# Kernel optimization log

Hardware: AMD Instinct MI355X
Metric: run time of the kernel (lower is better)

The kernel has to match this reference:

```python
import jax, jax.numpy as jnp
import numpy as np

# Grid parameters (from init_kwargs)
GRID_W, GRID_L, GRID_H = 96, 96, 48
VOXEL_SIZE = 0.05
MIN_POINTS_PER_VOXEL = 10


def setup_inputs() -> dict:
    key = jax.random.key(0)
    k1, k2 = jax.random.split(key, 2)
    # points uniform over a ~[0,1.5]^3 sub-volume so voxel occupancy is realistic
    point_coordinates = jax.random.uniform(k1, (4, 3, 480, 640), jnp.float32) * 1.5
    point_attributes = jax.random.normal(k2, (4, 16, 480, 640), jnp.float32)
    origin = jnp.zeros((4, 3), jnp.float32)
    return {"point_coordinates": point_coordinates,
            "point_attributes": point_attributes,
            "origin": origin}


def _voxelize_one(coords, attrs, org):
    # coords: [3, N], attrs: [C, N], org: [3]
    V = GRID_W * GRID_L * GRID_H
    bounds = jnp.array([GRID_W, GRID_L, GRID_H], jnp.int32)
    # per-point voxel index (floor == .long() for positive; OOB handled by mask)
    idx3 = jnp.floor((coords - org[:, None]) / VOXEL_SIZE).astype(jnp.int32)  # [3, N]
    in_bounds = jnp.all((idx3 >= 0) & (idx3 < bounds[:, None]), axis=0)       # [N]
    flat = idx3[0] * (GRID_L * GRID_H) + idx3[1] * GRID_H + idx3[2]           # [N]
    flat = jnp.where(in_bounds, flat, 0)  # route OOB points to voxel 0, masked out
    # occupancy: scatter-add of in-bounds mask
    counts = jax.ops.segment_sum(in_bounds.astype(jnp.float32), flat, num_segments=V)
    # max-pool of attributes per voxel; OOB points contribute -inf
    masked = jnp.where(in_bounds[None, :], attrs, -jnp.inf)                   # [C, N]
    vmax = jax.ops.segment_max(masked.T, flat, num_segments=V).T              # [C, V]
    occ = counts >= MIN_POINTS_PER_VOXEL                                      # [V]
    data = jnp.where(occ[None, :] & jnp.isfinite(vmax), vmax, 0.0)            # [C, V]
    return data, occ


def reference(point_coordinates, point_attributes, origin):
    b, c = point_attributes.shape[:2]
    coords = point_coordinates.reshape(b, 3, -1)   # [B, 3, N]
    attrs = point_attributes.reshape(b, c, -1)     # [B, C, N]
    data, occ = jax.vmap(_voxelize_one)(coords, attrs, origin)
    voxeldata = data.reshape(b, c, GRID_W, GRID_L, GRID_H)
    voxeloccupancy = occ.reshape(b, 1, GRID_W, GRID_L, GRID_H).astype(jnp.float32)
    return voxeldata, voxeloccupancy
```

## Files before the change

kernel.cpp:

```cpp
#include <hip/hip_runtime.h>
#include <cstdint>
#include <math.h>

#define GRID_W 96
#define GRID_L 96
#define GRID_H 48
#define NVOX (GRID_W * GRID_L * GRID_H)
#define VOXEL_SIZE 0.05f
#define MIN_PTS 10
#define BATCH 4
#define CHANS 16
#define NPTS (480 * 640)
#define TOTPTS (BATCH * NPTS)
#define TOTVOX (BATCH * NVOX)

#define SCAN_BLKS 864
#define SCAN_TPB 256
#define SCAN_EPT 8
#define SCAN_CHUNK (SCAN_TPB * SCAN_EPT)

#define ROWW 8

typedef unsigned nt_uint4  __attribute__((ext_vector_type(4)));
typedef float    nt_float4 __attribute__((ext_vector_type(4)));
typedef float    nt_float2 __attribute__((ext_vector_type(2)));

#define WS_OFFSETS 0
#define WS_VR      ((TOTVOX + 4) * 4)
#define WS_IDS     (WS_VR + TOTPTS * 4)
#define WS_ROWS    (WS_IDS + TOTPTS * 4 + 16)
#define WS_SUMS    (WS_ROWS + (size_t)TOTPTS * ROWW * 4)
#define WS_NEEDED  ((size_t)(WS_SUMS + 4096))

__device__ __forceinline__ unsigned bf16_rtne(float f) {
    unsigned u = __float_as_uint(f);
    return (u + 0x7FFFu + ((u >> 16) & 1u)) >> 16;
}
__device__ __forceinline__ unsigned pack2(float lo, float hi) {
    return bf16_rtne(lo) | (bf16_rtne(hi) << 16);
}



__global__ void k_pack(const float* __restrict__ attrs,
                       unsigned*    __restrict__ rows)
{
    int t = blockIdx.x * blockDim.x + threadIdx.x;
    if (t >= TOTPTS / 2) return;
    int pid = t * 2;
    int b = pid / NPTS;
    int n = pid - b * NPTS;

    const float* ab = attrs + (size_t)b * CHANS * NPTS + n;
    unsigned w[2][ROWW];
    #pragma unroll
    for (int c = 0; c < CHANS; c += 2) {
        nt_float2 a0 = __builtin_nontemporal_load((const nt_float2*)(ab + (size_t)c * NPTS));
        nt_float2 a1 = __builtin_nontemporal_load((const nt_float2*)(ab + (size_t)(c + 1) * NPTS));
        w[0][c >> 1] = pack2(a0.x, a1.x);
        w[1][c >> 1] = pack2(a0.y, a1.y);
    }
    uint4* dst = (uint4*)(rows + (size_t)pid * ROWW);
    dst[0] = uint4{w[0][0], w[0][1], w[0][2], w[0][3]};
    dst[1] = uint4{w[0][4], w[0][5], w[0][6], w[0][7]};
    dst[2] = uint4{w[1][0], w[1][1], w[1][2], w[1][3]};
    dst[3] = uint4{w[1][4], w[1][5], w[1][6], w[1][7]};
}

__global__ void k_vox(const float* __restrict__ coords,
                      const float* __restrict__ origin,
                      unsigned*    __restrict__ vr,
                      unsigned*    __restrict__ cnt)
{
    int t = blockIdx.x * blockDim.x + threadIdx.x;
    if (t >= TOTPTS / 4) return;
    int pid = t * 4;
    int b = pid / NPTS;
    int n = pid - b * NPTS;

    const float* cb = coords + (size_t)b * 3 * NPTS;
    nt_float4 X = __builtin_nontemporal_load((const nt_float4*)(cb + n));
    nt_float4 Y = __builtin_nontemporal_load((const nt_float4*)(cb + NPTS + n));
    nt_float4 Z = __builtin_nontemporal_load((const nt_float4*)(cb + 2 * NPTS + n));
    float ox = origin[b * 3 + 0];
    float oy = origin[b * 3 + 1];
    float oz = origin[b * 3 + 2];

    float xs[4] = {X.x, X.y, X.z, X.w};
    float ys[4] = {Y.x, Y.y, Y.z, Y.w};
    float zs[4] = {Z.x, Z.y, Z.z, Z.w};

    int  vv[4];
    bool ib[4];
    #pragma unroll
    for (int k = 0; k < 4; ++k) {
        int ix = (int)floorf((xs[k] - ox) / VOXEL_SIZE);
        int iy = (int)floorf((ys[k] - oy) / VOXEL_SIZE);
        int iz = (int)floorf((zs[k] - oz) / VOXEL_SIZE);
        ib[k] = ((unsigned)ix < GRID_W) & ((unsigned)iy < GRID_L) & ((unsigned)iz < GRID_H);
        vv[k] = b * NVOX + ix * (GRID_L * GRID_H) + iy * GRID_H + iz;
    }
    unsigned ps[4];
    #pragma unroll
    for (int k = 0; k < 4; ++k) {
        unsigned p = 0xFFFFFFFFu;
        if (ib[k]) {
            unsigned r = atomicAdd(&cnt[vv[k]], 1u);
            p = ((unsigned)vv[k] << 10) | (r & 1023u);
        }
        ps[k] = p;
    }
    *(uint4*)(vr + pid) = uint4{ps[0], ps[1], ps[2], ps[3]};
}

__global__ void k_scan1(unsigned* __restrict__ offsets,
                        unsigned* __restrict__ sums,
                        float*    __restrict__ occ)
{
    __shared__ unsigned s[SCAN_TPB];
    int t = threadIdx.x;
    int base = blockIdx.x * SCAN_CHUNK + t * SCAN_EPT;

    uint4 a = ((const uint4*)(offsets + base))[0];
    uint4 c = ((const uint4*)(offsets + base))[1];
    unsigned e[SCAN_EPT] = {a.x, a.y, a.z, a.w, c.x, c.y, c.z, c.w};

    nt_float4 oc0, oc1;
    oc0.x = (e[0] >= MIN_PTS) ? 1.f : 0.f;  oc0.y = (e[1] >= MIN_PTS) ? 1.f : 0.f;
    oc0.z = (e[2] >= MIN_PTS) ? 1.f : 0.f;  oc0.w = (e[3] >= MIN_PTS) ? 1.f : 0.f;
    oc1.x = (e[4] >= MIN_PTS) ? 1.f : 0.f;  oc1.y = (e[5] >= MIN_PTS) ? 1.f : 0.f;
    oc1.z = (e[6] >= MIN_PTS) ? 1.f : 0.f;  oc1.w = (e[7] >= MIN_PTS) ? 1.f : 0.f;
    __builtin_nontemporal_store(oc0, ((nt_float4*)(occ + base)));
    __builtin_nontemporal_store(oc1, ((nt_float4*)(occ + base)) + 1);

    unsigned tot = 0;
    #pragma unroll
    for (int k = 0; k < SCAN_EPT; ++k) { unsigned v = e[k]; e[k] = tot; tot += v; }

    s[t] = tot;
    __syncthreads();
    #pragma unroll
    for (int off = 1; off < SCAN_TPB; off <<= 1) {
        unsigned v = (t >= off) ? s[t - off] : 0u;
        __syncthreads();
        s[t] += v;
        __syncthreads();
    }
    unsigned prefix = s[t] - tot;
    #pragma unroll
    for (int k = 0; k < SCAN_EPT; ++k) e[k] += prefix;

    ((uint4*)(offsets + base))[0] = uint4{e[0], e[1], e[2], e[3]};
    ((uint4*)(offsets + base))[1] = uint4{e[4], e[5], e[6], e[7]};

    if (t == SCAN_TPB - 1) sums[blockIdx.x] = s[t];
}

__global__ void k_scan2(unsigned* __restrict__ sums) {
    __shared__ unsigned s[1024];
    int t = threadIdx.x;
    unsigned my = (t < SCAN_BLKS) ? sums[t] : 0u;
    s[t] = my;
    __syncthreads();
    #pragma unroll
    for (int off = 1; off < 1024; off <<= 1) {
        unsigned v = (t >= off) ? s[t - off] : 0u;
        __syncthreads();
        s[t] += v;
        __syncthreads();
    }
    if (t < SCAN_BLKS) sums[t] = s[t] - my;
    if (t == SCAN_BLKS - 1) sums[SCAN_BLKS] = s[t];
}

__global__ void k_scatter_ids4(const unsigned* __restrict__ vr,
                               const unsigned* __restrict__ offsets,
                               const unsigned* __restrict__ sums,
                               int*            __restrict__ ids)
{
    int t = blockIdx.x * blockDim.x + threadIdx.x;
    if (t >= TOTPTS / 4) return;
    int pid = t * 4;
    uint4 P = *(const uint4*)(vr + pid);
    unsigned ps[4] = {P.x, P.y, P.z, P.w};
    #pragma unroll
    for (int k = 0; k < 4; ++k) {
        if (ps[k] != 0xFFFFFFFFu) {
            unsigned v = ps[k] >> 10;
            unsigned pos = offsets[v] + sums[v >> 11] + (ps[k] & 1023u);
            ids[pos] = pid + k;
        }
    }
}

__global__ void k_gather_ind2(const unsigned* __restrict__ rows,
                              const int*      __restrict__ ids,
                              const unsigned* __restrict__ offsets,
                              const unsigned* __restrict__ sums,
                              float*          __restrict__ data)
{
    int g = blockIdx.x * blockDim.x + threadIdx.x;
    if (g >= TOTVOX / 2) return;
    int vox0 = g * 2;

    uint2 O = *(const uint2*)(offsets + vox0);
    unsigned base = sums[vox0 >> 11];
    unsigned s[3];
    s[0] = O.x + base;
    s[1] = O.y + base;
    s[2] = offsets[vox0 + 2] + sums[(vox0 + 2) >> 11];

    float m[2][CHANS];
    #pragma unroll
    for (int q = 0; q < 2; ++q) {
        unsigned k = s[q + 1] - s[q];
        unsigned s0 = s[q];
        if (k >= MIN_PTS) {
            const float ninf = -__builtin_inff();
            #pragma unroll
            for (int c = 0; c < CHANS; ++c) m[q][c] = ninf;
            unsigned j = 0;
            for (; j + 2 <= k; j += 2) {
                int p0 = ids[s0 + j];
                int p1 = ids[s0 + j + 1];
                const uint4* r0p = (const uint4*)(rows + (size_t)p0 * ROWW);
                const uint4* r1p = (const uint4*)(rows + (size_t)p1 * ROWW);
                uint4 l0 = r0p[0], h0 = r0p[1];
                uint4 l1 = r1p[0], h1 = r1p[1];
                unsigned wa[8] = {l0.x, l0.y, l0.z, l0.w, h0.x, h0.y, h0.z, h0.w};
                unsigned wb[8] = {l1.x, l1.y, l1.z, l1.w, h1.x, h1.y, h1.z, h1.w};
                #pragma unroll
                for (int h = 0; h < 8; ++h) {
                    m[q][2 * h]     = fmaxf(m[q][2 * h],
                                        fmaxf(__uint_as_float(wa[h] << 16),
                                              __uint_as_float(wb[h] << 16)));
                    m[q][2 * h + 1] = fmaxf(m[q][2 * h + 1],
                                        fmaxf(__uint_as_float(wa[h] & 0xFFFF0000u),
                                              __uint_as_float(wb[h] & 0xFFFF0000u)));
                }
            }
            if (j < k) {
                int p0 = ids[s0 + j];
                const uint4* r0p = (const uint4*)(rows + (size_t)p0 * ROWW);
                uint4 l0 = r0p[0], h0 = r0p[1];
                unsigned wa[8] = {l0.x, l0.y, l0.z, l0.w, h0.x, h0.y, h0.z, h0.w};
                #pragma unroll
                for (int h = 0; h < 8; ++h) {
                    m[q][2 * h]     = fmaxf(m[q][2 * h], __uint_as_float(wa[h] << 16));
                    m[q][2 * h + 1] = fmaxf(m[q][2 * h + 1],
                                            __uint_as_float(wa[h] & 0xFFFF0000u));
                }
            }
            #pragma unroll
            for (int c = 0; c < CHANS; ++c) if (!isfinite(m[q][c])) m[q][c] = 0.f;
        } else {
            #pragma unroll
            for (int c = 0; c < CHANS; ++c) m[q][c] = 0.f;
        }
    }

    int b = vox0 / NVOX;
    int v0 = vox0 - b * NVOX;
    float* db = data + (size_t)b * CHANS * NVOX + v0;
    #pragma unroll
    for (int c = 0; c < CHANS; ++c) {
        nt_float2 o = {m[0][c], m[1][c]};
        __builtin_nontemporal_store(o, (nt_float2*)(db + (size_t)c * NVOX));
    }
}


__device__ __forceinline__ unsigned flip_f32(float f) {
    unsigned u = __float_as_uint(f);
    unsigned mask = (unsigned)(-(int)(u >> 31)) | 0x80000000u;
    return u ^ mask;
}
__device__ __forceinline__ float unflip_f32(unsigned u) {
    unsigned mask = ((u >> 31) - 1u) | 0x80000000u;
    return __uint_as_float(u ^ mask);
}
#define FLIP_NEG_INF 0x007FFFFFu

__global__ void pv_init(uint4* __restrict__ out) {
    const int DATA4 = BATCH * CHANS * NVOX / 4;
    const int TOT4  = BATCH * (CHANS + 1) * NVOX / 4;
    int i = blockIdx.x * blockDim.x + threadIdx.x;
    if (i < TOT4) {
        unsigned val = (i < DATA4) ? FLIP_NEG_INF : 0u;
        out[i] = uint4{val, val, val, val};
    }
}

__global__ void pv_scatter(const float* __restrict__ coords,
                           const float* __restrict__ attrs,
                           const float* __restrict__ origin,
                           unsigned*    __restrict__ data_u,
                           unsigned*    __restrict__ cnt)
{
    int id = blockIdx.x * blockDim.x + threadIdx.x;
    if (id >= TOTPTS) return;
    int b = id / NPTS;
    int n = id - b * NPTS;
    const float* cb = coords + (size_t)b * 3 * NPTS;
    float x = cb[n], y = cb[NPTS + n], z = cb[2 * NPTS + n];
    float ox = origin[b * 3 + 0], oy = origin[b * 3 + 1], oz = origin[b * 3 + 2];
    int ix = (int)floorf((x - ox) / VOXEL_SIZE);
    int iy = (int)floorf((y - oy) / VOXEL_SIZE);
    int iz = (int)floorf((z - oz) / VOXEL_SIZE);
    if ((unsigned)ix < GRID_W && (unsigned)iy < GRID_L && (unsigned)iz < GRID_H) {
        int flat = ix * (GRID_L * GRID_H) + iy * GRID_H + iz;
        atomicAdd(&cnt[b * NVOX + flat], 1u);
        const float* ab = attrs + (size_t)b * CHANS * NPTS + n;
        unsigned*    db = data_u + (size_t)b * CHANS * NVOX + flat;
        #pragma unroll
        for (int c = 0; c < CHANS; ++c)
            atomicMax(&db[(size_t)c * NVOX], flip_f32(ab[(size_t)c * NPTS]));
    }
}

__global__ void pv_finalize(unsigned* __restrict__ data_u,
                            unsigned* __restrict__ cnt_u)
{
    int id = blockIdx.x * blockDim.x + threadIdx.x;
    if (id >= TOTVOX) return;
    int b = id / NVOX;
    int v = id - b * NVOX;
    unsigned cnt = cnt_u[id];
    bool occ = (cnt >= MIN_PTS);
    ((float*)cnt_u)[id] = occ ? 1.0f : 0.0f;
    unsigned* db = data_u + (size_t)b * CHANS * NVOX + v;
    #pragma unroll
    for (int c = 0; c < CHANS; ++c) {
        float f = unflip_f32(db[(size_t)c * NVOX]);
        ((float*)db)[(size_t)c * NVOX] = (occ && isfinite(f)) ? f : 0.0f;
    }
}


extern "C" void kernel_launch(void* const* d_in, const int* in_sizes, int n_in,
                              void* d_out, int out_size, void* d_ws, size_t ws_size,
                              hipStream_t stream) {
    const float* coords = (const float*)d_in[0];
    const float* attrs  = (const float*)d_in[1];
    const float* origin = (const float*)d_in[2];

    float* out = (float*)d_out;
    float* data = out;
    float* occ  = out + (size_t)BATCH * CHANS * NVOX;

    if (ws_size >= WS_NEEDED) {
        char* ws = (char*)d_ws;
        unsigned* offsets = (unsigned*)(ws + WS_OFFSETS);
        unsigned* vr      = (unsigned*)(ws + WS_VR);
        int*      ids     = (int*)(ws + WS_IDS);
        unsigned* rows    = (unsigned*)(ws + WS_ROWS);
        unsigned* sums    = (unsigned*)(ws + WS_SUMS);

        (void)hipMemsetAsync(offsets, 0, (size_t)(TOTVOX + 4) * 4, stream);
        k_vox<<<(TOTPTS / 4 + 255) / 256, 256, 0, stream>>>(coords, origin, vr, offsets);
        k_pack<<<(TOTPTS / 2 + 255) / 256, 256, 0, stream>>>(attrs, rows);
        k_scan1<<<SCAN_BLKS, SCAN_TPB, 0, stream>>>(offsets, sums, occ);
        k_scan2<<<1, 1024, 0, stream>>>(sums);
        k_scatter_ids4<<<(TOTPTS / 4 + 255) / 256, 256, 0, stream>>>(vr, offsets, sums, ids);
        k_gather_ind2<<<(TOTVOX / 2 + 255) / 256, 256, 0, stream>>>(rows, ids, offsets, sums, data);
    } else {
        unsigned* data_u = (unsigned*)data;
        unsigned* cnt    = (unsigned*)occ;
        const int TOT4 = BATCH * (CHANS + 1) * NVOX / 4;
        pv_init<<<(TOT4 + 255) / 256, 256, 0, stream>>>((uint4*)d_out);
        pv_scatter<<<(TOTPTS + 255) / 256, 256, 0, stream>>>(coords, attrs, origin, data_u, cnt);
        pv_finalize<<<(TOTVOX + 255) / 256, 256, 0, stream>>>(data_u, cnt);
    }
}
```

Baseline: 298.8 us.

## Fuse voxel-count and attribute-pack kernels; replicate counters to spread atomic contention

Merges the voxel-index/count kernel and the bf16 attribute-pack kernel into one launch, split by block index, so the two independent passes can run concurrently and one launch is saved. Voxel occupancy counters are replicated four ways, one copy per point slot within a thread, which spreads same-address atomic contention. The scan kernel sums the four replicas and the id scatter adds a prefix over the lower replicas to recover each point's slot. The cost is a memset four times larger, extra counter reads in the scan and scatter kernels, and a rank field that grows to 11 bits.

Measured after the change: 308.0 us. 3.1% more time.

```diff
diff --git a/kernel.cpp b/kernel.cpp
--- a/kernel.cpp
+++ b/kernel.cpp
@@ -20,13 +20,18 @@
 #define SCAN_CHUNK (SCAN_TPB * SCAN_EPT)
 
 #define ROWW 8
+#define NREP 4
+
+#define VOX_BLKS  (TOTPTS / 4 / 256)
+#define PACK_BLKS (TOTPTS / 2 / 256)
 
 typedef unsigned nt_uint4  __attribute__((ext_vector_type(4)));
 typedef float    nt_float4 __attribute__((ext_vector_type(4)));
 typedef float    nt_float2 __attribute__((ext_vector_type(2)));
 
 #define WS_OFFSETS 0
-#define WS_VR      ((TOTVOX + 4) * 4)
+#define WS_CNT4    ((TOTVOX + 4) * 4)
+#define WS_VR      (WS_CNT4 + NREP * TOTVOX * 4)
 #define WS_IDS     (WS_VR + TOTPTS * 4)
 #define WS_ROWS    (WS_IDS + TOTPTS * 4 + 16)
 #define WS_SUMS    (WS_ROWS + (size_t)TOTPTS * ROWW * 4)
@@ -41,89 +46,94 @@
 }
 
 
-
-__global__ void k_pack(const float* __restrict__ attrs,
-                       unsigned*    __restrict__ rows)
-{
-    int t = blockIdx.x * blockDim.x + threadIdx.x;
-    if (t >= TOTPTS / 2) return;
-    int pid = t * 2;
-    int b = pid / NPTS;
-    int n = pid - b * NPTS;
-
-    const float* ab = attrs + (size_t)b * CHANS * NPTS + n;
-    unsigned w[2][ROWW];
-    #pragma unroll
-    for (int c = 0; c < CHANS; c += 2) {
-        nt_float2 a0 = __builtin_nontemporal_load((const nt_float2*)(ab + (size_t)c * NPTS));
-        nt_float2 a1 = __builtin_nontemporal_load((const nt_float2*)(ab + (size_t)(c + 1) * NPTS));
-        w[0][c >> 1] = pack2(a0.x, a1.x);
-        w[1][c >> 1] = pack2(a0.y, a1.y);
-    }
-    uint4* dst = (uint4*)(rows + (size_t)pid * ROWW);
-    dst[0] = uint4{w[0][0], w[0][1], w[0][2], w[0][3]};
-    dst[1] = uint4{w[0][4], w[0][5], w[0][6], w[0][7]};
-    dst[2] = uint4{w[1][0], w[1][1], w[1][2], w[1][3]};
-    dst[3] = uint4{w[1][4], w[1][5], w[1][6], w[1][7]};
-}
-
-__global__ void k_vox(const float* __restrict__ coords,
-                      const float* __restrict__ origin,
-                      unsigned*    __restrict__ vr,
-                      unsigned*    __restrict__ cnt)
-{
-    int t = blockIdx.x * blockDim.x + threadIdx.x;
-    if (t >= TOTPTS / 4) return;
-    int pid = t * 4;
-    int b = pid / NPTS;
-    int n = pid - b * NPTS;
-
-    const float* cb = coords + (size_t)b * 3 * NPTS;
-    nt_float4 X = __builtin_nontemporal_load((const nt_float4*)(cb + n));
-    nt_float4 Y = __builtin_nontemporal_load((const nt_float4*)(cb + NPTS + n));
-    nt_float4 Z = __builtin_nontemporal_load((const nt_float4*)(cb + 2 * NPTS + n));
-    float ox = origin[b * 3 + 0];
-    float oy = origin[b * 3 + 1];
-    float oz = origin[b * 3 + 2];
-
-    float xs[4] = {X.x, X.y, X.z, X.w};
-    float ys[4] = {Y.x, Y.y, Y.z, Y.w};
-    float zs[4] = {Z.x, Z.y, Z.z, Z.w};
-
-    int  vv[4];
-    bool ib[4];
-    #pragma unroll
-    for (int k = 0; k < 4; ++k) {
-        int ix = (int)floorf((xs[k] - ox) / VOXEL_SIZE);
-        int iy = (int)floorf((ys[k] - oy) / VOXEL_SIZE);
-        int iz = (int)floorf((zs[k] - oz) / VOXEL_SIZE);
-        ib[k] = ((unsigned)ix < GRID_W) & ((unsigned)iy < GRID_L) & ((unsigned)iz < GRID_H);
-        vv[k] = b * NVOX + ix * (GRID_L * GRID_H) + iy * GRID_H + iz;
-    }
-    unsigned ps[4];
-    #pragma unroll
-    for (int k = 0; k < 4; ++k) {
-        unsigned p = 0xFFFFFFFFu;
-        if (ib[k]) {
-            unsigned r = atomicAdd(&cnt[vv[k]], 1u);
-            p = ((unsigned)vv[k] << 10) | (r & 1023u);
-        }
-        ps[k] = p;
-    }
-    *(uint4*)(vr + pid) = uint4{ps[0], ps[1], ps[2], ps[3]};
-}
-
-__global__ void k_scan1(unsigned* __restrict__ offsets,
-                        unsigned* __restrict__ sums,
-                        float*    __restrict__ occ)
+__global__ void k_front(const float* __restrict__ coords,
+                        const float* __restrict__ attrs,
+                        const float* __restrict__ origin,
+                        unsigned*    __restrict__ vr,
+                        unsigned*    __restrict__ rows,
+                        unsigned*    __restrict__ cnt4)
+{
+    if (blockIdx.x < VOX_BLKS) {
+        int t = blockIdx.x * blockDim.x + threadIdx.x;
+        int pid = t * 4;
+        int b = pid / NPTS;
+        int n = pid - b * NPTS;
+
+        const float* cb = coords + (size_t)b * 3 * NPTS;
+        nt_float4 X = __builtin_nontemporal_load((const nt_float4*)(cb + n));
+        nt_float4 Y = __builtin_nontemporal_load((const nt_float4*)(cb + NPTS + n));
+        nt_float4 Z = __builtin_nontemporal_load((const nt_float4*)(cb + 2 * NPTS + n));
+        float ox = origin[b * 3 + 0];
+        float oy = origin[b * 3 + 1];
+        float oz = origin[b * 3 + 2];
+
+        float xs[4] = {X.x, X.y, X.z, X.w};
+        float ys[4] = {Y.x, Y.y, Y.z, Y.w};
+        float zs[4] = {Z.x, Z.y, Z.z, Z.w};
+
+        int  vv[4];
+        bool ib[4];
+        #pragma unroll
+        for (int k = 0; k < 4; ++k) {
+            int ix = (int)floorf((xs[k] - ox) / VOXEL_SIZE);
+            int iy = (int)floorf((ys[k] - oy) / VOXEL_SIZE);
+            int iz = (int)floorf((zs[k] - oz) / VOXEL_SIZE);
+            ib[k] = ((unsigned)ix < GRID_W) & ((unsigned)iy < GRID_L) & ((unsigned)iz < GRID_H);
+            vv[k] = b * NVOX + ix * (GRID_L * GRID_H) + iy * GRID_H + iz;
+        }
+        unsigned ps[4];
+        #pragma unroll
+        for (int k = 0; k < 4; ++k) {
+            unsigned p = 0xFFFFFFFFu;
+            if (ib[k]) {
+                unsigned r = atomicAdd(&cnt4[(size_t)k * TOTVOX + vv[k]], 1u);
+                p = ((unsigned)vv[k] << 11) | (r & 2047u);
+            }
+            ps[k] = p;
+        }
+        *(uint4*)(vr + pid) = uint4{ps[0], ps[1], ps[2], ps[3]};
+    } else {
+        int t = (blockIdx.x - VOX_BLKS) * blockDim.x + threadIdx.x;
+        if (t >= TOTPTS / 2) return;
+        int pid = t * 2;
+        int b = pid / NPTS;
+        int n = pid - b * NPTS;
+
+        const float* ab = attrs + (size_t)b * CHANS * NPTS + n;
+        unsigned w[2][ROWW];
+        #pragma unroll
+        for (int c = 0; c < CHANS; c += 2) {
+            nt_float2 a0 = __builtin_nontemporal_load((const nt_float2*)(ab + (size_t)c * NPTS));
+            nt_float2 a1 = __builtin_nontemporal_load((const nt_float2*)(ab + (size_t)(c + 1) * NPTS));
+            w[0][c >> 1] = pack2(a0.x, a1.x);
+            w[1][c >> 1] = pack2(a0.y, a1.y);
+        }
+        uint4* dst = (uint4*)(rows + (size_t)pid * ROWW);
+        dst[0] = uint4{w[0][0], w[0][1], w[0][2], w[0][3]};
+        dst[1] = uint4{w[0][4], w[0][5], w[0][6], w[0][7]};
+        dst[2] = uint4{w[1][0], w[1][1], w[1][2], w[1][3]};
+        dst[3] = uint4{w[1][4], w[1][5], w[1][6], w[1][7]};
+    }
+}
+
+__global__ void k_scan1(const unsigned* __restrict__ cnt4,
+                        unsigned*       __restrict__ offsets,
+                        unsigned*       __restrict__ sums,
+                        float*          __restrict__ occ)
 {
     __shared__ unsigned s[SCAN_TPB];
     int t = threadIdx.x;
     int base = blockIdx.x * SCAN_CHUNK + t * SCAN_EPT;
 
-    uint4 a = ((const uint4*)(offsets + base))[0];
-    uint4 c = ((const uint4*)(offsets + base))[1];
-    unsigned e[SCAN_EPT] = {a.x, a.y, a.z, a.w, c.x, c.y, c.z, c.w};
+    unsigned e[SCAN_EPT] = {0, 0, 0, 0, 0, 0, 0, 0};
+    #pragma unroll
+    for (int r = 0; r < NREP; ++r) {
+        const uint4* p = (const uint4*)(cnt4 + (size_t)r * TOTVOX + base);
+        uint4 a = p[0];
+        uint4 c = p[1];
+        e[0] += a.x; e[1] += a.y; e[2] += a.z; e[3] += a.w;
+        e[4] += c.x; e[5] += c.y; e[6] += c.z; e[7] += c.w;
+    }
 
     nt_float4 oc0, oc1;
     oc0.x = (e[0] >= MIN_PTS) ? 1.f : 0.f;  oc0.y = (e[1] >= MIN_PTS) ? 1.f : 0.f;
@@ -174,6 +184,7 @@
 }
 
 __global__ void k_scatter_ids4(const unsigned* __restrict__ vr,
+                               const unsigned* __restrict__ cnt4,
                                const unsigned* __restrict__ offsets,
                                const unsigned* __restrict__ sums,
                                int*            __restrict__ ids)
@@ -186,8 +197,12 @@
     #pragma unroll
     for (int k = 0; k < 4; ++k) {
         if (ps[k] != 0xFFFFFFFFu) {
-            unsigned v = ps[k] >> 10;
-            unsigned pos = offsets[v] + sums[v >> 11] + (ps[k] & 1023u);
+            unsigned v = ps[k] >> 11;
+            unsigned sub = 0;
+            #pragma unroll
+            for (int r2 = 0; r2 < 4; ++r2)
+                if (r2 < k) sub += cnt4[(size_t)r2 * TOTVOX + v];
+            unsigned pos = offsets[v] + sums[v >> 11] + sub + (ps[k] & 2047u);
             ids[pos] = pid + k;
         }
     }
@@ -351,18 +366,22 @@
     if (ws_size >= WS_NEEDED) {
         char* ws = (char*)d_ws;
         unsigned* offsets = (unsigned*)(ws + WS_OFFSETS);
+        unsigned* cnt4    = (unsigned*)(ws + WS_CNT4);
         unsigned* vr      = (unsigned*)(ws + WS_VR);
         int*      ids     = (int*)(ws + WS_IDS);
         unsigned* rows    = (unsigned*)(ws + WS_ROWS);
         unsigned* sums    = (unsigned*)(ws + WS_SUMS);
 
-        (void)hipMemsetAsync(offsets, 0, (size_t)(TOTVOX + 4) * 4, stream);
-        k_vox<<<(TOTPTS / 4 + 255) / 256, 256, 0, stream>>>(coords, origin, vr, offsets);
-        k_pack<<<(TOTPTS / 2 + 255) / 256, 256, 0, stream>>>(attrs, rows);
-        k_scan1<<<SCAN_BLKS, SCAN_TPB, 0, stream>>>(offsets, sums, occ);
+        (void)hipMemsetAsync(cnt4, 0, (size_t)NREP * TOTVOX * 4, stream);
+        (void)hipMemsetAsync(offsets + TOTVOX, 0, 16, stream);
+        k_front<<<VOX_BLKS + PACK_BLKS, 256, 0, stream>>>(coords, attrs, origin,
+                                                          vr, rows, cnt4);
+        k_scan1<<<SCAN_BLKS, SCAN_TPB, 0, stream>>>(cnt4, offsets, sums, occ);
         k_scan2<<<1, 1024, 0, stream>>>(sums);
-        k_scatter_ids4<<<(TOTPTS / 4 + 255) / 256, 256, 0, stream>>>(vr, offsets, sums, ids);
-        k_gather_ind2<<<(TOTVOX / 2 + 255) / 256, 256, 0, stream>>>(rows, ids, offsets, sums, data);
+        k_scatter_ids4<<<(TOTPTS / 4 + 255) / 256, 256, 0, stream>>>(vr, cnt4, offsets,
+                                                                     sums, ids);
+        k_gather_ind2<<<(TOTVOX / 2 + 255) / 256, 256, 0, stream>>>(rows, ids, offsets,
+                                                                    sums, data);
     } else {
         unsigned* data_u = (unsigned*)data;
         unsigned* cnt    = (unsigned*)occ;
```

## Scatter packed attribute rows into voxel-sorted order, removing the id indirection

Applied to the files above, without the earlier changes.

Fuses the bf16 attribute packing into the scatter pass. Each point's packed 32-byte row is now written directly to its counting-sort position instead of writing only a point id. The gather kernel then reads each voxel's rows contiguously with nontemporal loads, dropping the separate pack kernel, the ids array and the random row gathers. The cost is random 32-byte writes in the scatter kernel in place of random 4-byte id writes, and the gather no longer has a pid-ordered rows buffer to draw on.

Measured after the change: 339.9 us. 13.8% more time.

```diff
diff --git a/kernel.cpp b/kernel.cpp
--- a/kernel.cpp
+++ b/kernel.cpp
@@ -27,9 +27,8 @@
 
 #define WS_OFFSETS 0
 #define WS_VR      ((TOTVOX + 4) * 4)
-#define WS_IDS     (WS_VR + TOTPTS * 4)
-#define WS_ROWS    (WS_IDS + TOTPTS * 4 + 16)
-#define WS_SUMS    (WS_ROWS + (size_t)TOTPTS * ROWW * 4)
+#define WS_SROWS   (WS_VR + TOTPTS * 4 + 16)
+#define WS_SUMS    (WS_SROWS + (size_t)TOTPTS * ROWW * 4)
 #define WS_NEEDED  ((size_t)(WS_SUMS + 4096))
 
 __device__ __forceinline__ unsigned bf16_rtne(float f) {
@@ -42,35 +41,10 @@
 
 
 
-__global__ void k_pack(const float* __restrict__ attrs,
-                       unsigned*    __restrict__ rows)
-{
-    int t = blockIdx.x * blockDim.x + threadIdx.x;
-    if (t >= TOTPTS / 2) return;
-    int pid = t * 2;
-    int b = pid / NPTS;
-    int n = pid - b * NPTS;
-
-    const float* ab = attrs + (size_t)b * CHANS * NPTS + n;
-    unsigned w[2][ROWW];
-    #pragma unroll
-    for (int c = 0; c < CHANS; c += 2) {
-        nt_float2 a0 = __builtin_nontemporal_load((const nt_float2*)(ab + (size_t)c * NPTS));
-        nt_float2 a1 = __builtin_nontemporal_load((const nt_float2*)(ab + (size_t)(c + 1) * NPTS));
-        w[0][c >> 1] = pack2(a0.x, a1.x);
-        w[1][c >> 1] = pack2(a0.y, a1.y);
-    }
-    uint4* dst = (uint4*)(rows + (size_t)pid * ROWW);
-    dst[0] = uint4{w[0][0], w[0][1], w[0][2], w[0][3]};
-    dst[1] = uint4{w[0][4], w[0][5], w[0][6], w[0][7]};
-    dst[2] = uint4{w[1][0], w[1][1], w[1][2], w[1][3]};
-    dst[3] = uint4{w[1][4], w[1][5], w[1][6], w[1][7]};
-}
-
-__global__ void k_vox(const float* __restrict__ coords,
-                      const float* __restrict__ origin,
-                      unsigned*    __restrict__ vr,
-                      unsigned*    __restrict__ cnt)
+__global__ void k_hist(const float* __restrict__ coords,
+                       const float* __restrict__ origin,
+                       unsigned*    __restrict__ vr,
+                       unsigned*    __restrict__ cnt)
 {
     int t = blockIdx.x * blockDim.x + threadIdx.x;
     if (t >= TOTPTS / 4) return;
@@ -173,28 +147,47 @@
     if (t == SCAN_BLKS - 1) sums[SCAN_BLKS] = s[t];
 }
 
-__global__ void k_scatter_ids4(const unsigned* __restrict__ vr,
+__global__ void k_scatter_rows(const unsigned* __restrict__ vr,
+                               const float*    __restrict__ attrs,
                                const unsigned* __restrict__ offsets,
                                const unsigned* __restrict__ sums,
-                               int*            __restrict__ ids)
+                               unsigned*       __restrict__ srows)
 {
     int t = blockIdx.x * blockDim.x + threadIdx.x;
     if (t >= TOTPTS / 4) return;
     int pid = t * 4;
+    int b = pid / NPTS;
+    int n = pid - b * NPTS;
+
     uint4 P = *(const uint4*)(vr + pid);
     unsigned ps[4] = {P.x, P.y, P.z, P.w};
+
+    const float* ab = attrs + (size_t)b * CHANS * NPTS + n;
+    unsigned w[4][ROWW];
+    #pragma unroll
+    for (int c = 0; c < CHANS; c += 2) {
+        nt_float4 a0 = __builtin_nontemporal_load((const nt_float4*)(ab + (size_t)c * NPTS));
+        nt_float4 a1 = __builtin_nontemporal_load((const nt_float4*)(ab + (size_t)(c + 1) * NPTS));
+        w[0][c >> 1] = pack2(a0.x, a1.x);
+        w[1][c >> 1] = pack2(a0.y, a1.y);
+        w[2][c >> 1] = pack2(a0.z, a1.z);
+        w[3][c >> 1] = pack2(a0.w, a1.w);
+    }
+
     #pragma unroll
     for (int k = 0; k < 4; ++k) {
-        if (ps[k] != 0xFFFFFFFFu) {
-            unsigned v = ps[k] >> 10;
-            unsigned pos = offsets[v] + sums[v >> 11] + (ps[k] & 1023u);
-            ids[pos] = pid + k;
+        unsigned p = ps[k];
+        if (p != 0xFFFFFFFFu) {
+            unsigned v   = p >> 10;
+            unsigned pos = offsets[v] + sums[v >> 11] + (p & 1023u);
+            uint4* d = (uint4*)(srows + (size_t)pos * ROWW);
+            d[0] = uint4{w[k][0], w[k][1], w[k][2], w[k][3]};
+            d[1] = uint4{w[k][4], w[k][5], w[k][6], w[k][7]};
         }
     }
 }
 
-__global__ void k_gather_ind2(const unsigned* __restrict__ rows,
-                              const int*      __restrict__ ids,
+__global__ void k_gather_seq2(const unsigned* __restrict__ srows,
                               const unsigned* __restrict__ offsets,
                               const unsigned* __restrict__ sums,
                               float*          __restrict__ data)
@@ -221,12 +214,11 @@
             for (int c = 0; c < CHANS; ++c) m[q][c] = ninf;
             unsigned j = 0;
             for (; j + 2 <= k; j += 2) {
-                int p0 = ids[s0 + j];
-                int p1 = ids[s0 + j + 1];
-                const uint4* r0p = (const uint4*)(rows + (size_t)p0 * ROWW);
-                const uint4* r1p = (const uint4*)(rows + (size_t)p1 * ROWW);
-                uint4 l0 = r0p[0], h0 = r0p[1];
-                uint4 l1 = r1p[0], h1 = r1p[1];
+                const nt_uint4* rp = (const nt_uint4*)(srows + (size_t)(s0 + j) * ROWW);
+                nt_uint4 l0 = __builtin_nontemporal_load(rp);
+                nt_uint4 h0 = __builtin_nontemporal_load(rp + 1);
+                nt_uint4 l1 = __builtin_nontemporal_load(rp + 2);
+                nt_uint4 h1 = __builtin_nontemporal_load(rp + 3);
                 unsigned wa[8] = {l0.x, l0.y, l0.z, l0.w, h0.x, h0.y, h0.z, h0.w};
                 unsigned wb[8] = {l1.x, l1.y, l1.z, l1.w, h1.x, h1.y, h1.z, h1.w};
                 #pragma unroll
@@ -240,9 +232,9 @@
                 }
             }
             if (j < k) {
-                int p0 = ids[s0 + j];
-                const uint4* r0p = (const uint4*)(rows + (size_t)p0 * ROWW);
-                uint4 l0 = r0p[0], h0 = r0p[1];
+                const nt_uint4* rp = (const nt_uint4*)(srows + (size_t)(s0 + j) * ROWW);
+                nt_uint4 l0 = __builtin_nontemporal_load(rp);
+                nt_uint4 h0 = __builtin_nontemporal_load(rp + 1);
                 unsigned wa[8] = {l0.x, l0.y, l0.z, l0.w, h0.x, h0.y, h0.z, h0.w};
                 #pragma unroll
                 for (int h = 0; h < 8; ++h) {
@@ -352,17 +344,17 @@
         char* ws = (char*)d_ws;
         unsigned* offsets = (unsigned*)(ws + WS_OFFSETS);
         unsigned* vr      = (unsigned*)(ws + WS_VR);
-        int*      ids     = (int*)(ws + WS_IDS);
-        unsigned* rows    = (unsigned*)(ws + WS_ROWS);
+        unsigned* srows   = (unsigned*)(ws + WS_SROWS);
         unsigned* sums    = (unsigned*)(ws + WS_SUMS);
 
         (void)hipMemsetAsync(offsets, 0, (size_t)(TOTVOX + 4) * 4, stream);
-        k_vox<<<(TOTPTS / 4 + 255) / 256, 256, 0, stream>>>(coords, origin, vr, offsets);
-        k_pack<<<(TOTPTS / 2 + 255) / 256, 256, 0, stream>>>(attrs, rows);
+        k_hist<<<(TOTPTS / 4 + 255) / 256, 256, 0, stream>>>(coords, origin, vr, offsets);
         k_scan1<<<SCAN_BLKS, SCAN_TPB, 0, stream>>>(offsets, sums, occ);
         k_scan2<<<1, 1024, 0, stream>>>(sums);
-        k_scatter_ids4<<<(TOTPTS / 4 + 255) / 256, 256, 0, stream>>>(vr, offsets, sums, ids);
-        k_gather_ind2<<<(TOTVOX / 2 + 255) / 256, 256, 0, stream>>>(rows, ids, offsets, sums, data);
+        k_scatter_rows<<<(TOTPTS / 4 + 255) / 256, 256, 0, stream>>>(vr, attrs, offsets,
+                                                                     sums, srows);
+        k_gather_seq2<<<(TOTVOX / 2 + 255) / 256, 256, 0, stream>>>(srows, offsets,
+                                                                    sums, data);
     } else {
         unsigned* data_u = (unsigned*)data;
         unsigned* cnt    = (unsigned*)occ;
```
